# Performance work log

Hardware: AMD Instinct MI355X
Metric: run time of the kernel (lower is better)

## Reference

```python
import jax, jax.numpy as jnp
import numpy as np

N = 100000
E = 600000
IN_DIM = 128
OUT_DIM = 256
BN_EPS = 1e-5


def setup_inputs() -> dict:
    key = jax.random.key(0)
    ks = jax.random.split(key, 12)
    x = jax.random.normal(ks[0], (N, IN_DIM), dtype=jnp.float32)
    edge_index = jax.random.randint(ks[1], (2, E), 0, N, dtype=jnp.int64)
    s1 = 1.0 / np.sqrt(IN_DIM)
    s2 = 1.0 / np.sqrt(OUT_DIM)
    return {
        "x": x,
        "edge_index": edge_index,
        "eps": jnp.zeros((), dtype=jnp.float32),  # GINConv eps init = 0
        "W1": jax.random.uniform(ks[2], (IN_DIM, OUT_DIM), jnp.float32, -s1, s1),
        "b1": jnp.zeros((OUT_DIM,), jnp.float32),
        "W2": jax.random.uniform(ks[3], (OUT_DIM, OUT_DIM), jnp.float32, -s2, s2),
        "b2": jnp.zeros((OUT_DIM,), jnp.float32),
        "gamma": jnp.ones((OUT_DIM,), jnp.float32),
        "beta": jnp.zeros((OUT_DIM,), jnp.float32),
        "run_mean": jnp.zeros((OUT_DIM,), jnp.float32),
        "run_var": jnp.ones((OUT_DIM,), jnp.float32),
        "Wp": jax.random.uniform(ks[4], (IN_DIM, OUT_DIM), jnp.float32, -s1, s1),
        "bp": jnp.zeros((OUT_DIM,), jnp.float32),
    }


def reference(x, edge_index, eps, W1, b1, W2, b2, gamma, beta, run_mean, run_var, Wp, bp):
    src, dst = edge_index[0], edge_index[1]
    # GIN aggregation: sum_{j in N(i)} x_j  (scatter-add of source features to dst)
    agg = jax.ops.segment_sum(x[src], dst, num_segments=N)
    h = (1.0 + eps) * x + agg            # [N, in_dim]
    # 2-layer MLP (nn1)
    h = jax.nn.relu(h @ W1 + b1) @ W2 + b2   # [N, out_dim]
    # BatchNorm1d (eval mode: running stats); dropout = identity (eval)
    h = (h - run_mean) * jax.lax.rsqrt(run_var + BN_EPS) * gamma + beta
    # residual with projection (in_dim != out_dim)
    return h + x @ Wp + bp
```

## Files before the change

### kernel.cpp

```cpp
#include <hip/hip_runtime.h>

#define N_ 100000
#define E_ 600000
#define IND_ 128
#define OUTD_ 256
#define NT_ (N_/16)
#define NB_ 98
#define CASTN_ (N_*IND_/2)

typedef __attribute__((ext_vector_type(8))) short bf16x8;
typedef __attribute__((ext_vector_type(4))) float f32x4;
typedef __attribute__((ext_vector_type(2))) unsigned int u32x2;

static __device__ __forceinline__ unsigned f2bf_u(float f){
  union { float f; unsigned u; } v; v.f = f;
  return (v.u + 0x7fffu + ((v.u >> 16) & 1u)) >> 16;
}
static __device__ __forceinline__ unsigned pack2(float a, float b){
  return f2bf_u(a) | (f2bf_u(b) << 16);
}
static __device__ __forceinline__ float blo(unsigned u){
  union { unsigned u; float f; } v; v.u = u << 16; return v.f;
}
static __device__ __forceinline__ float bhi(unsigned u){
  union { unsigned u; float f; } v; v.u = u & 0xffff0000u; return v.f;
}

__global__ void k_prep(const float* __restrict__ x,
                       const float* __restrict__ W1, const float* __restrict__ W2,
                       const float* __restrict__ Wp, const float* __restrict__ b2,
                       const float* __restrict__ gamma, const float* __restrict__ beta,
                       const float* __restrict__ mean, const float* __restrict__ var,
                       const float* __restrict__ bp,
                       const int* __restrict__ dst, int* __restrict__ deg,
                       unsigned short* __restrict__ W1s, unsigned short* __restrict__ W2s,
                       unsigned short* __restrict__ Wps,
                       float* __restrict__ scale, float* __restrict__ shift,
                       unsigned* __restrict__ xbw)
{
  int gid = blockIdx.x*256 + threadIdx.x;
  if (gid < 16384) {
    const float* W; unsigned short* Ws; int u;
    if (gid < 4096)       { W = W1; Ws = W1s; u = gid; }
    else if (gid < 12288) { W = W2; Ws = W2s; u = gid - 4096; }
    else                  { W = Wp; Ws = Wps; u = gid - 12288; }
    int l  = u & 63;
    int km = (u >> 6) & 1;
    int t  = (u >> 7) & 15;
    int q  = u >> 11;
    int kk = 2*q + km;
    int kb = kk*32 + (l >> 4)*8;
    int c  = 16*t + (l & 15);
    #pragma unroll
    for (int j = 0; j < 8; j++)
      Ws[u*8 + j] = (unsigned short)f2bf_u(W[(size_t)(kb + j)*OUTD_ + c]);
  } else if (gid < 16640) {
    int c = gid - 16384;
    float s = gamma[c] * rsqrtf(var[c] + 1e-5f);
    scale[c] = s;
    shift[c] = (b2[c] - mean[c]) * s + beta[c] + bp[c];
  } else if (gid < 16640 + CASTN_) {
    int ci = gid - 16640;
    float2 v = ((const float2*)x)[ci];
    xbw[ci] = pack2(v.x, v.y);
  } else if (gid < 16640 + CASTN_ + E_) {
    int e = gid - 16640 - CASTN_;
    atomicAdd(&deg[dst[e]], 1);
  }
}

__global__ __launch_bounds__(1024) void k_scan1(const int* __restrict__ deg,
                                                int* __restrict__ bsum, int* __restrict__ offs){
  __shared__ int red[16];
  int tid = threadIdx.x;
  int i = blockIdx.x*1024 + tid;
  int v = (i < N_) ? deg[i] : 0;
  #pragma unroll
  for (int d = 32; d; d >>= 1) v += __shfl_down(v, d);
  if ((tid & 63) == 0) red[tid >> 6] = v;
  __syncthreads();
  if (tid < 16) {
    int s = red[tid];
    #pragma unroll
    for (int d = 8; d; d >>= 1) s += __shfl_down(s, d, 16);
    if (tid == 0) bsum[blockIdx.x] = s;
  }
  if (blockIdx.x == 0 && tid == 0) offs[N_] = E_;
}

__global__ __launch_bounds__(1024) void k_scan2(const int* __restrict__ deg,
                                                const int* __restrict__ bsum, int* __restrict__ offs){
  __shared__ int bs[128];
  __shared__ int d1[1024];
  int tid = threadIdx.x;
  if (tid < 128) bs[tid] = (tid < NB_) ? bsum[tid] : 0;
  __syncthreads();
  #pragma unroll
  for (int d = 1; d < 128; d <<= 1){
    int v = (tid < 128 && tid >= d) ? bs[tid - d] : 0;
    __syncthreads();
    if (tid < 128) bs[tid] += v;
    __syncthreads();
  }
  int bprefix = (blockIdx.x > 0) ? bs[blockIdx.x - 1] : 0;
  int i = blockIdx.x*1024 + tid;
  int v = (i < N_) ? deg[i] : 0;
  d1[tid] = v;
  __syncthreads();
  #pragma unroll
  for (int d = 1; d < 1024; d <<= 1){
    int t = (tid >= d) ? d1[tid - d] : 0;
    __syncthreads();
    d1[tid] += t;
    __syncthreads();
  }
  if (i < N_) offs[i] = bprefix + d1[tid] - v;
}

__global__ void k_fill(const int* __restrict__ src, const int* __restrict__ dst,
                       const int* __restrict__ offs, int* __restrict__ cur, int* __restrict__ adj){
  int e = blockIdx.x*256 + threadIdx.x;
  if (e < E_) {
    int d = dst[e];
    int p = atomicAdd(&cur[d], 1);
    adj[offs[d] + p] = src[e];
  }
}

__global__ void k_agg(const unsigned* __restrict__ xb32, const int* __restrict__ offs,
                      const int* __restrict__ adj, const float* __restrict__ epsp,
                      unsigned* __restrict__ h0)
{
  int row  = blockIdx.x*4 + (threadIdx.x >> 6);
  int lane = threadIdx.x & 63;
  if (row >= N_) return;
  unsigned xw = xb32[(size_t)row*64 + lane];
  float ax0=0,ay0=0,ax1=0,ay1=0,ax2=0,ay2=0,ax3=0,ay3=0;
  float ax4=0,ay4=0,ax5=0,ay5=0,ax6=0,ay6=0,ax7=0,ay7=0;
  int b = offs[row], e = offs[row+1];
  for (int base = b; base < e; base += 64){
    int cnt = min(64, e - base);
    int idx = adj[base + min(lane, cnt - 1)];
    int j = 0;
    for (; j + 8 <= cnt; j += 8){
      int n0 = __shfl(idx, j+0), n1 = __shfl(idx, j+1);
      int n2 = __shfl(idx, j+2), n3 = __shfl(idx, j+3);
      int n4 = __shfl(idx, j+4), n5 = __shfl(idx, j+5);
      int n6 = __shfl(idx, j+6), n7 = __shfl(idx, j+7);
      unsigned v0 = xb32[(size_t)n0*64 + lane];
      unsigned v1 = xb32[(size_t)n1*64 + lane];
      unsigned v2 = xb32[(size_t)n2*64 + lane];
      unsigned v3 = xb32[(size_t)n3*64 + lane];
      unsigned v4 = xb32[(size_t)n4*64 + lane];
      unsigned v5 = xb32[(size_t)n5*64 + lane];
      unsigned v6 = xb32[(size_t)n6*64 + lane];
      unsigned v7 = xb32[(size_t)n7*64 + lane];
      ax0 += blo(v0); ay0 += bhi(v0);
      ax1 += blo(v1); ay1 += bhi(v1);
      ax2 += blo(v2); ay2 += bhi(v2);
      ax3 += blo(v3); ay3 += bhi(v3);
      ax4 += blo(v4); ay4 += bhi(v4);
      ax5 += blo(v5); ay5 += bhi(v5);
      ax6 += blo(v6); ay6 += bhi(v6);
      ax7 += blo(v7); ay7 += bhi(v7);
    }
    for (; j < cnt; j++){
      int n = __shfl(idx, j);
      unsigned v = xb32[(size_t)n*64 + lane];
      ax0 += blo(v); ay0 += bhi(v);
    }
  }
  float ax = ((ax0+ax1)+(ax2+ax3)) + ((ax4+ax5)+(ax6+ax7));
  float ay = ((ay0+ay1)+(ay2+ay3)) + ((ay4+ay5)+(ay6+ay7));
  float k1 = 1.f + epsp[0];
  h0[(size_t)row*64 + lane] = pack2(fmaf(k1, blo(xw), ax), fmaf(k1, bhi(xw), ay));
}

__global__ __launch_bounds__(256) void k_mlp1(const unsigned short* __restrict__ h0,
        const bf16x8* __restrict__ W1s, const float* __restrict__ b1,
        unsigned short* __restrict__ h1s)
{
  __shared__ bf16x8 w[2048];
  __shared__ __align__(16) char trans[4][2][1280];
  int tid = threadIdx.x;
  int wv = tid >> 6, lane = tid & 63, g = lane >> 4, r = lane & 15;
  int tile0 = blockIdx.x*4 + wv;
  int tile  = min(tile0, NT_ - 1);

  const bf16x8* hrow = (const bf16x8*)(h0 + ((size_t)tile*16 + r)*IND_);
  bf16x8 B[4];
  #pragma unroll
  for (int kk = 0; kk < 4; kk++) B[kk] = hrow[kk*4 + g];

  f32x4 acc[16];
  #pragma unroll
  for (int t = 0; t < 16; t++) acc[t] = (f32x4){0.f,0.f,0.f,0.f};

  for (int q = 0; q < 2; q++){
    __syncthreads();
    #pragma unroll
    for (int i = 0; i < 8; i++) w[tid + i*256] = W1s[q*2048 + tid + i*256];
    __syncthreads();
    #pragma unroll
    for (int km = 0; km < 2; km++){
      bf16x8 Bf = B[2*q + km];
      #pragma unroll
      for (int t = 0; t < 16; t++)
        acc[t] = __builtin_amdgcn_mfma_f32_16x16x32_bf16(w[(t*2+km)*64 + lane], Bf, acc[t], 0,0,0);
    }
  }

  const float4* b1v = (const float4*)b1;
  unsigned short* outp = h1s + (size_t)tile*4096;
  bool act = (tile0 < NT_);
  #pragma unroll
  for (int kkh = 0; kkh < 8; kkh++){
    char* tr = &trans[wv][kkh & 1][0];
    #pragma unroll
    for (int h = 0; h < 2; h++){
      int t = 2*kkh + h;
      float4 bb = b1v[t*4 + g];
      f32x4 a = acc[t];
      float v0 = fmaxf(a.x + bb.x, 0.f);
      float v1 = fmaxf(a.y + bb.y, 0.f);
      float v2 = fmaxf(a.z + bb.z, 0.f);
      float v3 = fmaxf(a.w + bb.w, 0.f);
      u32x2 dd; dd.x = pack2(v0, v1); dd.y = pack2(v2, v3);
      *(u32x2*)(tr + r*80 + h*32 + g*8) = dd;
    }
    bf16x8 frag = *(const bf16x8*)(tr + r*80 + g*16);
    if (act) *(bf16x8*)(outp + (kkh*64 + lane)*8) = frag;
  }
}

__global__ __launch_bounds__(256) void k_mlp2(const bf16x8* __restrict__ h1s,
        const unsigned short* __restrict__ xb16,
        const bf16x8* __restrict__ W2s, const bf16x8* __restrict__ Wps,
        const float* __restrict__ scale, const float* __restrict__ shift,
        float* __restrict__ out)
{
  __shared__ bf16x8 w[2048];
  int tid = threadIdx.x, wv = tid >> 6, lane = tid & 63, g = lane >> 4, r = lane & 15;
  int tile0 = blockIdx.x*4 + wv;
  int tile  = min(tile0, NT_ - 1);
  const bf16x8* h1f  = h1s + (size_t)tile*512;
  const bf16x8* xrow = (const bf16x8*)(xb16 + ((size_t)tile*16 + r)*IND_);

  f32x4 acc[16];
  #pragma unroll
  for (int t = 0; t < 16; t++) acc[t] = (f32x4){0.f,0.f,0.f,0.f};

  for (int q = 0; q < 4; q++){
    __syncthreads();
    #pragma unroll
    for (int i = 0; i < 8; i++) w[tid + i*256] = W2s[q*2048 + tid + i*256];
    __syncthreads();
    #pragma unroll
    for (int km = 0; km < 2; km++){
      bf16x8 Bf = h1f[(2*q + km)*64 + lane];
      #pragma unroll
      for (int t = 0; t < 16; t++)
        acc[t] = __builtin_amdgcn_mfma_f32_16x16x32_bf16(w[(t*2+km)*64 + lane], Bf, acc[t], 0,0,0);
    }
  }
  for (int q = 0; q < 2; q++){
    __syncthreads();
    #pragma unroll
    for (int i = 0; i < 8; i++) w[tid + i*256] = Wps[q*2048 + tid + i*256];
    __syncthreads();
    #pragma unroll
    for (int km = 0; km < 2; km++){
      bf16x8 Bf = xrow[(2*q + km)*4 + g];
      #pragma unroll
      for (int t = 0; t < 16; t++)
        acc[t] = __builtin_amdgcn_mfma_f32_16x16x32_bf16(w[(t*2+km)*64 + lane], Bf, acc[t], 0,0,0);
    }
  }

  if (tile0 < NT_){
    const float4* sc = (const float4*)scale;
    const float4* sh = (const float4*)shift;
    #pragma unroll
    for (int t = 0; t < 16; t++){
      float4 s = sc[t*4 + g], b = sh[t*4 + g];
      f32x4 a = acc[t];
      float4 o;
      o.x = fmaf(a.x, s.x, b.x);
      o.y = fmaf(a.y, s.y, b.y);
      o.z = fmaf(a.z, s.z, b.z);
      o.w = fmaf(a.w, s.w, b.w);
      *(float4*)(out + ((size_t)tile*16 + r)*OUTD_ + t*16 + g*4) = o;
    }
  }
}

extern "C" void kernel_launch(void* const* d_in, const int* in_sizes, int n_in,
                              void* d_out, int out_size, void* d_ws, size_t ws_size,
                              hipStream_t stream)
{
  const float* x     = (const float*)d_in[0];
  const int*   ei    = (const int*)d_in[1];
  const float* eps   = (const float*)d_in[2];
  const float* W1    = (const float*)d_in[3];
  const float* b1    = (const float*)d_in[4];
  const float* W2    = (const float*)d_in[5];
  const float* b2    = (const float*)d_in[6];
  const float* gamma = (const float*)d_in[7];
  const float* beta  = (const float*)d_in[8];
  const float* rmean = (const float*)d_in[9];
  const float* rvar  = (const float*)d_in[10];
  const float* Wp    = (const float*)d_in[11];
  const float* bp    = (const float*)d_in[12];
  float* out = (float*)d_out;

  char* ws = (char*)d_ws; size_t off = 0;
  auto carve = [&](size_t b)->char* { char* p = ws + off; off = (off + b + 255) & ~(size_t)255; return p; };
  unsigned*       xbuf  = (unsigned*)carve((size_t)CASTN_*4);
  unsigned*       h0    = (unsigned*)carve((size_t)N_*64*4);
  unsigned short* h1s   = (unsigned short*)carve((size_t)N_*OUTD_*2);
  unsigned short* W1s   = (unsigned short*)carve(4096*16);
  unsigned short* W2s   = (unsigned short*)carve(8192*16);
  unsigned short* Wps   = (unsigned short*)carve(4096*16);
  float*          scale = (float*)carve(256*4);
  float*          shift = (float*)carve(256*4);
  int*            deg   = (int*)carve((size_t)N_*4);
  int*            cur   = (int*)carve((size_t)N_*4);
  int*            offs  = (int*)carve((size_t)(N_+1)*4);
  int*            adj   = (int*)carve((size_t)E_*4);
  int*            bsum  = (int*)carve((size_t)NB_*4);

  hipMemsetAsync(deg, 0, (size_t)N_*4, stream);
  hipMemsetAsync(cur, 0, (size_t)N_*4, stream);

  k_prep <<<(16640 + CASTN_ + E_ + 255)/256, 256, 0, stream>>>(x, W1, W2, Wp, b2, gamma, beta,
                                  rmean, rvar, bp, ei + E_, deg,
                                  W1s, W2s, Wps, scale, shift, xbuf);
  k_scan1<<<NB_, 1024, 0, stream>>>(deg, bsum, offs);
  k_scan2<<<NB_, 1024, 0, stream>>>(deg, bsum, offs);
  k_fill <<<(E_+255)/256, 256, 0, stream>>>(ei, ei + E_, offs, cur, adj);
  k_agg  <<<(N_+3)/4, 256, 0, stream>>>(xbuf, offs, adj, eps, h0);
  k_mlp1 <<<(NT_+3)/4, 256, 0, stream>>>((const unsigned short*)h0, (const bf16x8*)W1s, b1, h1s);
  k_mlp2 <<<(NT_+3)/4, 256, 0, stream>>>((const bf16x8*)h1s, (const unsigned short*)xbuf,
                                         (const bf16x8*)W2s, (const bf16x8*)Wps, scale, shift, out);
}
```

Before: 209.9 us.

## Fuse MLP layer kernels, keeping hidden activations in registers

New measurement: 267.4 us. 1.27x slower.

```diff
diff --git a/kernel.cpp b/kernel.cpp
--- a/kernel.cpp
+++ b/kernel.cpp
@@ -176,9 +176,12 @@
   h0[(size_t)row*64 + lane] = pack2(fmaf(k1, blo(xw), ax), fmaf(k1, bhi(xw), ay));
 }
 
-__global__ __launch_bounds__(256) void k_mlp1(const unsigned short* __restrict__ h0,
+__global__ __launch_bounds__(256) void k_mlp(const unsigned short* __restrict__ h0,
+        const unsigned short* __restrict__ xb16,
         const bf16x8* __restrict__ W1s, const float* __restrict__ b1,
-        unsigned short* __restrict__ h1s)
+        const bf16x8* __restrict__ W2s, const bf16x8* __restrict__ Wps,
+        const float* __restrict__ scale, const float* __restrict__ shift,
+        float* __restrict__ out)
 {
   __shared__ bf16x8 w[2048];
   __shared__ __align__(16) char trans[4][2][1280];
@@ -188,9 +191,12 @@
   int tile  = min(tile0, NT_ - 1);
 
   const bf16x8* hrow = (const bf16x8*)(h0 + ((size_t)tile*16 + r)*IND_);
-  bf16x8 B[4];
+  const bf16x8* xrow = (const bf16x8*)(xb16 + ((size_t)tile*16 + r)*IND_);
+  bf16x8 B[4], XV[4];
   #pragma unroll
   for (int kk = 0; kk < 4; kk++) B[kk] = hrow[kk*4 + g];
+  #pragma unroll
+  for (int kk = 0; kk < 4; kk++) XV[kk] = xrow[kk*4 + g];
 
   f32x4 acc[16];
   #pragma unroll
@@ -211,8 +217,7 @@
   }
 
   const float4* b1v = (const float4*)b1;
-  unsigned short* outp = h1s + (size_t)tile*4096;
-  bool act = (tile0 < NT_);
+  bf16x8 H[8];
   #pragma unroll
   for (int kkh = 0; kkh < 8; kkh++){
     char* tr = &trans[wv][kkh & 1][0];
@@ -228,25 +233,9 @@
       u32x2 dd; dd.x = pack2(v0, v1); dd.y = pack2(v2, v3);
       *(u32x2*)(tr + r*80 + h*32 + g*8) = dd;
     }
-    bf16x8 frag = *(const bf16x8*)(tr + r*80 + g*16);
-    if (act) *(bf16x8*)(outp + (kkh*64 + lane)*8) = frag;
-  }
-}
-
-__global__ __launch_bounds__(256) void k_mlp2(const bf16x8* __restrict__ h1s,
-        const unsigned short* __restrict__ xb16,
-        const bf16x8* __restrict__ W2s, const bf16x8* __restrict__ Wps,
-        const float* __restrict__ scale, const float* __restrict__ shift,
-        float* __restrict__ out)
-{
-  __shared__ bf16x8 w[2048];
-  int tid = threadIdx.x, wv = tid >> 6, lane = tid & 63, g = lane >> 4, r = lane & 15;
-  int tile0 = blockIdx.x*4 + wv;
-  int tile  = min(tile0, NT_ - 1);
-  const bf16x8* h1f  = h1s + (size_t)tile*512;
-  const bf16x8* xrow = (const bf16x8*)(xb16 + ((size_t)tile*16 + r)*IND_);
-
-  f32x4 acc[16];
+    H[kkh] = *(const bf16x8*)(tr + r*80 + g*16);
+  }
+
   #pragma unroll
   for (int t = 0; t < 16; t++) acc[t] = (f32x4){0.f,0.f,0.f,0.f};
 
@@ -257,7 +246,7 @@
     __syncthreads();
     #pragma unroll
     for (int km = 0; km < 2; km++){
-      bf16x8 Bf = h1f[(2*q + km)*64 + lane];
+      bf16x8 Bf = H[2*q + km];
       #pragma unroll
       for (int t = 0; t < 16; t++)
         acc[t] = __builtin_amdgcn_mfma_f32_16x16x32_bf16(w[(t*2+km)*64 + lane], Bf, acc[t], 0,0,0);
@@ -270,7 +259,7 @@
     __syncthreads();
     #pragma unroll
     for (int km = 0; km < 2; km++){
-      bf16x8 Bf = xrow[(2*q + km)*4 + g];
+      bf16x8 Bf = XV[2*q + km];
       #pragma unroll
       for (int t = 0; t < 16; t++)
         acc[t] = __builtin_amdgcn_mfma_f32_16x16x32_bf16(w[(t*2+km)*64 + lane], Bf, acc[t], 0,0,0);
@@ -317,7 +306,6 @@
   auto carve = [&](size_t b)->char* { char* p = ws + off; off = (off + b + 255) & ~(size_t)255; return p; };
   unsigned*       xbuf  = (unsigned*)carve((size_t)CASTN_*4);
   unsigned*       h0    = (unsigned*)carve((size_t)N_*64*4);
-  unsigned short* h1s   = (unsigned short*)carve((size_t)N_*OUTD_*2);
   unsigned short* W1s   = (unsigned short*)carve(4096*16);
   unsigned short* W2s   = (unsigned short*)carve(8192*16);
   unsigned short* Wps   = (unsigned short*)carve(4096*16);
@@ -339,7 +327,7 @@
   k_scan2<<<NB_, 1024, 0, stream>>>(deg, bsum, offs);
   k_fill <<<(E_+255)/256, 256, 0, stream>>>(ei, ei + E_, offs, cur, adj);
   k_agg  <<<(N_+3)/4, 256, 0, stream>>>(xbuf, offs, adj, eps, h0);
-  k_mlp1 <<<(NT_+3)/4, 256, 0, stream>>>((const unsigned short*)h0, (const bf16x8*)W1s, b1, h1s);
-  k_mlp2 <<<(NT_+3)/4, 256, 0, stream>>>((const bf16x8*)h1s, (const unsigned short*)xbuf,
-                                         (const bf16x8*)W2s, (const bf16x8*)Wps, scale, shift, out);
-}
+  k_mlp  <<<(NT_+3)/4, 256, 0, stream>>>((const unsigned short*)h0, (const unsigned short*)xbuf,
+                                         (const bf16x8*)W1s, b1, (const bf16x8*)W2s,
+                                         (const bf16x8*)Wps, scale, shift, out);
+}
```
